# Performance work log

Hardware: AMD Instinct MI355X
Metric: run time of the kernel (lower is better)

Reference implementation:

```python
import jax, jax.numpy as jnp
import numpy as np

B, N = 4, 2048
NUM_SHAPES = 16
EPS = 1e-5


def _angle(u, v):
    # u, v: [b, 3, n] -> angle via atan2(||u x v||, u.v), standard PPF angle
    s = jnp.linalg.norm(jnp.cross(u, v, axis=1), axis=1)
    c = jnp.sum(u * v, axis=1)
    return jnp.arctan2(s, c)


def _ppf(p1, p2, n1, n2):
    d = p2 - p1  # [b,3,n]
    return jnp.stack([_angle(n1, d), _angle(n2, d), _angle(n1, n2),
                      jnp.linalg.norm(d, axis=1)], axis=1)  # [b,4,n]


def _smlp(x, w, g, b):
    # 1x1 Conv1d (no bias; absorbed by BN) + BatchNorm1d (batch stats) + ReLU
    y = jnp.einsum('oc,bcn->bon', w, x)
    mu = y.mean(axis=(0, 2), keepdims=True)
    var = jnp.mean((y - mu) ** 2, axis=(0, 2), keepdims=True)
    y = (y - mu) * jax.lax.rsqrt(var + EPS) * g[None, :, None] + b[None, :, None]
    return jax.nn.relu(y)


def _forward(inputs, pf0_w, pf0_g, pf0_b, pf1_w, pf1_g, pf1_b,
             pf2_w, pf2_g, pf2_b, pf3_w, pf3_g, pf3_b,
             cls0_w, cls0_g, cls0_b, cls1_w, cls1_g, cls1_b,
             cls2_w, cls2_g, cls2_b, cls3_w, cls3_bias):
    one_hot = inputs[:, -NUM_SHAPES:, :]
    coords = inputs[:, :3, :]
    n = coords.shape[2]
    normals = inputs[:, 3:6, :]
    normals = normals / jnp.linalg.norm(normals, axis=1, keepdims=True)

    cc = coords.mean(axis=2, keepdims=True)          # [b,3,1]
    cn = normals.mean(axis=2, keepdims=True)         # [b,3,1]
    ncn = cn / jnp.linalg.norm(cn, axis=1, keepdims=True)

    old_ppfs = _ppf(jnp.broadcast_to(cc, coords.shape), coords,
                    jnp.broadcast_to(cn, coords.shape), normals)  # [b,4,n]

    nc = coords - cc
    dot = jnp.sum(nc * ncn, axis=1, keepdims=True)   # [b,1,n]
    proj = nc - dot * cn                              # [b,3,n] (unnormalized cn, as in source)
    P = proj.transpose(0, 2, 1)                       # [b,n,3]

    cos_a = jnp.einsum('bic,bjc->bij', P, P)          # [b,n,n]
    sin_a = jnp.linalg.norm(jnp.cross(P[:, :, None, :], P[:, None, :, :]), axis=-1)
    at = jnp.arctan2(sin_a, cos_a)
    at = jnp.where(at <= 1e-5, jnp.float32(100.0), at)
    # torch.median -> lower median: sorted index (n-1)//2
    alpha = jnp.sort(at, axis=2)[:, :, (n - 1) // 2]  # [b,n]

    feats = jnp.concatenate([old_ppfs, alpha[:, None, :]], axis=1)  # [b,5,n]

    outs = [one_hot]
    f = feats
    for w, g, b in [(pf0_w, pf0_g, pf0_b), (pf1_w, pf1_g, pf1_b),
                    (pf2_w, pf2_g, pf2_b), (pf3_w, pf3_g, pf3_b)]:
        f = _smlp(f, w, g, b)
        outs.append(f)
    outs.append(jnp.broadcast_to(jnp.max(f, axis=-1, keepdims=True), f.shape))
    x = jnp.concatenate(outs, axis=1)                 # [b,2384,n]

    for w, g, b in [(cls0_w, cls0_g, cls0_b), (cls1_w, cls1_g, cls1_b),
                    (cls2_w, cls2_g, cls2_b)]:
        x = _smlp(x, w, g, b)
    return jnp.einsum('oc,bcn->bon', cls3_w, x) + cls3_bias[None, :, None]


def setup_inputs() -> dict:
    key = jax.random.key(0)
    ks = jax.random.split(key, 12)
    inp = {"inputs": jax.random.normal(ks[0], (B, 3 + 3 + NUM_SHAPES, N), jnp.float32)}
    pf_dims = [(5, 64), (64, 128), (128, 128), (128, 1024)]
    for i, (ci, co) in enumerate(pf_dims):
        inp[f"pf{i}_w"] = jax.random.normal(ks[1 + i], (co, ci), jnp.float32) / np.sqrt(ci).astype(np.float32)
        inp[f"pf{i}_g"] = jnp.ones((co,), jnp.float32)
        inp[f"pf{i}_b"] = jnp.zeros((co,), jnp.float32)
    cls_dims = [(2384, 256), (256, 256), (256, 128)]
    for j, (ci, co) in enumerate(cls_dims):
        inp[f"cls{j}_w"] = jax.random.normal(ks[6 + j], (co, ci), jnp.float32) / np.sqrt(ci).astype(np.float32)
        inp[f"cls{j}_g"] = jnp.ones((co,), jnp.float32)
        inp[f"cls{j}_b"] = jnp.zeros((co,), jnp.float32)
    inp["cls3_w"] = jax.random.normal(ks[10], (50, 128), jnp.float32) / np.sqrt(128).astype(np.float32)
    inp["cls3_bias"] = jnp.zeros((50,), jnp.float32)
    return inp


def reference(inputs, pf0_w, pf0_g, pf0_b, pf1_w, pf1_g, pf1_b,
              pf2_w, pf2_g, pf2_b, pf3_w, pf3_g, pf3_b,
              cls0_w, cls0_g, cls0_b, cls1_w, cls1_g, cls1_b,
              cls2_w, cls2_g, cls2_b, cls3_w, cls3_bias):
    return _forward(inputs, pf0_w, pf0_g, pf0_b, pf1_w, pf1_g, pf1_b,
                    pf2_w, pf2_g, pf2_b, pf3_w, pf3_g, pf3_b,
                    cls0_w, cls0_g, cls0_b, cls1_w, cls1_g, cls1_b,
                    cls2_w, cls2_g, cls2_b, cls3_w, cls3_bias)
```

## Files before the change

### kernel.cpp

```cpp
#include <hip/hip_runtime.h>
#include <math.h>

#define BB 4
#define NN 2048
#define MM 8192
#define EPSF 1e-5f
#define LDC 1376

typedef _Float16 half8 __attribute__((ext_vector_type(8)));
typedef float f32x4 __attribute__((ext_vector_type(4)));

__device__ __forceinline__ unsigned short f2h(float x) {
    _Float16 h = (_Float16)x;
    return __builtin_bit_cast(unsigned short, h);
}
__device__ __forceinline__ float h2f(unsigned short u) {
    return (float)__builtin_bit_cast(_Float16, u);
}
__device__ __forceinline__ unsigned fflip(float x) {
    unsigned u = __builtin_bit_cast(unsigned, x);
    return (u >> 31) ? ~u : (u | 0x80000000u);
}
__device__ __forceinline__ float funflip(unsigned s) {
    unsigned u = (s >> 31) ? (s ^ 0x80000000u) : ~s;
    return __builtin_bit_cast(float, u);
}
#define FLIP_NEG_INF 0x007FFFFFu

__device__ __forceinline__ int wave_sum_dpp(int v) {
    v += __builtin_amdgcn_update_dpp(0, v, 0x111, 0xF, 0xF, true);
    v += __builtin_amdgcn_update_dpp(0, v, 0x112, 0xF, 0xF, true);
    v += __builtin_amdgcn_update_dpp(0, v, 0x114, 0xF, 0xF, true);
    v += __builtin_amdgcn_update_dpp(0, v, 0x118, 0xF, 0xF, true);
    v += __builtin_amdgcn_update_dpp(0, v, 0x142, 0xa, 0xF, true);
    v += __builtin_amdgcn_update_dpp(0, v, 0x143, 0xc, 0xF, true);
    return __builtin_amdgcn_readlane(v, 63);
}

__device__ __forceinline__ float angle3(float ux, float uy, float uz,
                                        float vx, float vy, float vz) {
    float crx = uy * vz - uz * vy;
    float cry = uz * vx - ux * vz;
    float crz = ux * vy - uy * vx;
    float s = sqrtf(crx * crx + cry * cry + crz * crz);
    float c = ux * vx + uy * vy + uz * vz;
    return atan2f(s, c);
}

__device__ __forceinline__ void bncoef(const float* __restrict__ sums,
                                       const float* __restrict__ g,
                                       const float* __restrict__ bb,
                                       int o, float& a, float& c) {
    float mu = sums[o] * (1.f / 8192.f);
    float var = sums[1024 + o] * (1.f / 8192.f) - mu * mu;
    var = fmaxf(var, 0.f);
    a = g[o] * (1.0f / sqrtf(var + EPSF));
    c = bb[o] - mu * a;
}

__global__ __launch_bounds__(256) void prep_k(const float* __restrict__ in,
                                              const float* __restrict__ w1, const float* __restrict__ w2,
                                              const float* __restrict__ w3, const float* __restrict__ w4,
                                              const float* __restrict__ w5, const float* __restrict__ w6,
                                              const float* __restrict__ w7,
                                              unsigned short* __restrict__ Wb,
                                              float* __restrict__ st,
                                              unsigned* __restrict__ zp,
                                              unsigned short* __restrict__ XCb) {
    int blk = blockIdx.x;
    int t = threadIdx.x;
    if (blk < 864) {
        int idx0 = blk * 1024 + t * 4;
        ushort4 r;
        unsigned short* rp = (unsigned short*)&r;
        #pragma unroll
        for (int e = 0; e < 4; ++e) {
            int idx = idx0 + e;
            unsigned short v;
            if (idx < 8192) v = f2h(w1[idx]);
            else if (idx < 24576) v = f2h(w2[idx - 8192]);
            else if (idx < 155648) v = f2h(w3[idx - 24576]);
            else if (idx < 507904) {
                int l = idx - 155648;
                int o = l / 1376, k = l - o * 1376;
                v = (k < 1360) ? f2h(w4[o * 2384 + k]) : (unsigned short)0;
            } else if (idx < 573440) v = f2h(w5[idx - 507904]);
            else if (idx < 606208) v = f2h(w6[idx - 573440]);
            else if (idx < 614400) {
                int l = idx - 606208;
                int o = l >> 7, k = l & 127;
                v = (o < 50) ? f2h(w7[o * 128 + k]) : (unsigned short)0;
            } else {
                int l = idx - 614400;
                int c = l >> 8, o = l & 255;
                v = (c < 1024) ? f2h(w4[o * 2384 + 1360 + c]) : (unsigned short)0;
            }
            rp[e] = v;
        }
        *(ushort4*)&Wb[idx0] = r;
    } else if (blk < 868) {
        int b = blk - 864;
        const float* base = in + (size_t)b * 22 * NN;
        float cs0 = 0.f, cs1 = 0.f, cs2 = 0.f, ns0 = 0.f, ns1 = 0.f, ns2 = 0.f;
        for (int n = t; n < NN; n += 256) {
            float cx = base[0 * NN + n], cy = base[1 * NN + n], cz = base[2 * NN + n];
            float nx = base[3 * NN + n], ny = base[4 * NN + n], nz = base[5 * NN + n];
            float inv = 1.0f / sqrtf(nx * nx + ny * ny + nz * nz);
            cs0 += cx; cs1 += cy; cs2 += cz;
            ns0 += nx * inv; ns1 += ny * inv; ns2 += nz * inv;
        }
        __shared__ float red[6][256];
        red[0][t] = cs0; red[1][t] = cs1; red[2][t] = cs2;
        red[3][t] = ns0; red[4][t] = ns1; red[5][t] = ns2;
        __syncthreads();
        for (int s = 128; s > 0; s >>= 1) {
            if (t < s) {
                #pragma unroll
                for (int i = 0; i < 6; ++i) red[i][t] += red[i][t + s];
            }
            __syncthreads();
        }
        if (t == 0) {
            float ccx = red[0][0] / (float)NN, ccy = red[1][0] / (float)NN, ccz = red[2][0] / (float)NN;
            float cnx = red[3][0] / (float)NN, cny = red[4][0] / (float)NN, cnz = red[5][0] / (float)NN;
            float inv = 1.0f / sqrtf(cnx * cnx + cny * cny + cnz * cnz);
            float* s9 = st + b * 16;
            s9[0] = ccx; s9[1] = ccy; s9[2] = ccz;
            s9[3] = cnx; s9[4] = cny; s9[5] = cnz;
            s9[6] = cnx * inv; s9[7] = cny * inv; s9[8] = cnz * inv;
        }
    } else if (blk < 944) {
        int idx = (blk - 868) * 256 + t;
        zp[idx] = (idx >= 14336 && idx < 18432) ? FLIP_NEG_INF : 0u;
    } else {
        int m = (blk - 944) * 256 + t;
        int b = m >> 11, n = m & (NN - 1);
        const float* src = in + (size_t)b * 22 * NN + 6 * NN + n;
        unsigned short vals[16];
        #pragma unroll
        for (int r = 0; r < 16; ++r) vals[r] = f2h(src[(size_t)r * NN]);
        ushort4* dst = (ushort4*)&XCb[(size_t)m * LDC];
        #pragma unroll
        for (int q = 0; q < 4; ++q)
            dst[q] = make_ushort4(vals[4 * q], vals[4 * q + 1], vals[4 * q + 2], vals[4 * q + 3]);
        ushort4 z = make_ushort4(0, 0, 0, 0);
        ushort4* pz = (ushort4*)&XCb[(size_t)m * LDC + 1360];
        pz[0] = z; pz[1] = z; pz[2] = z; pz[3] = z;
    }
}

__global__ __launch_bounds__(256) void point_k(const float* __restrict__ in,
                                               const float* __restrict__ st,
                                               float4* __restrict__ PQ,
                                               float* __restrict__ F0) {
    int idx = blockIdx.x * 256 + threadIdx.x;
    int b = idx >> 11, n = idx & (NN - 1);
    const float* base = in + (size_t)b * 22 * NN;
    const float* s9 = st + b * 16;
    float cx = base[0 * NN + n], cy = base[1 * NN + n], cz = base[2 * NN + n];
    float nx = base[3 * NN + n], ny = base[4 * NN + n], nz = base[5 * NN + n];
    float inv = 1.0f / sqrtf(nx * nx + ny * ny + nz * nz);
    nx *= inv; ny *= inv; nz *= inv;
    float ccx = s9[0], ccy = s9[1], ccz = s9[2];
    float cnx = s9[3], cny = s9[4], cnz = s9[5];
    float ex = s9[6], ey = s9[7], ez = s9[8];
    float dx = cx - ccx, dy = cy - ccy, dz = cz - ccz;
    F0[0 * MM + idx] = angle3(cnx, cny, cnz, dx, dy, dz);
    F0[1 * MM + idx] = angle3(nx, ny, nz, dx, dy, dz);
    F0[2 * MM + idx] = angle3(cnx, cny, cnz, nx, ny, nz);
    F0[3 * MM + idx] = sqrtf(dx * dx + dy * dy + dz * dz);
    float dot = dx * ex + dy * ey + dz * ez;
    float px = dx - dot * cnx;
    float py = dy - dot * cny;
    float pz = dz - dot * cnz;
    PQ[idx] = make_float4(px, py, pz, sqrtf(px * px + py * py + pz * pz));
}

__global__ __launch_bounds__(256) void alpha_k(const float4* __restrict__ PQ,
                                               float* __restrict__ F0) {
    int row = blockIdx.x * 4 + (threadIdx.x >> 6);
    int lane = threadIdx.x & 63;
    int b = row >> 11;
    const float4* base = PQ + (size_t)b * NN;
    float4 a = base[row & (NN - 1)];
    unsigned u[16];
    #pragma unroll
    for (int c = 0; c < 4; ++c) {
        #pragma unroll
        for (int j = 0; j < 4; ++j) {
            int s2 = c * 8 + j * 2;
            float4 bv0 = base[s2 * 64 + lane];
            float4 bv1 = base[(s2 + 1) * 64 + lane];
            float k0, k1;
            {
                float cx = a.y * bv0.z - a.z * bv0.y;
                float cy = a.z * bv0.x - a.x * bv0.z;
                float cz = a.x * bv0.y - a.y * bv0.x;
                float ss = cx * cx + cy * cy + cz * cz;
                float dc = a.x * bv0.x + a.y * bv0.y + a.z * bv0.z;
                float den = dc + a.w * bv0.w;
                float rc = __builtin_amdgcn_rcpf(den);
                k0 = ss * rc * rc;
                if (k0 <= 2.5e-11f) k0 = __builtin_inff();
            }
            {
                float cx = a.y * bv1.z - a.z * bv1.y;
                float cy = a.z * bv1.x - a.x * bv1.z;
                float cz = a.x * bv1.y - a.y * bv1.x;
                float ss = cx * cx + cy * cy + cz * cz;
                float dc = a.x * bv1.x + a.y * bv1.y + a.z * bv1.z;
                float den = dc + a.w * bv1.w;
                float rc = __builtin_amdgcn_rcpf(den);
                k1 = ss * rc * rc;
                if (k1 <= 2.5e-11f) k1 = __builtin_inff();
            }
            u[c * 4 + j] = (unsigned)f2h(k0) | ((unsigned)f2h(k1) << 16);
        }
        asm volatile("" ::: "memory");
    }
    unsigned T = 0u;
    for (int bit = 14; bit >= 0; --bit) {
        unsigned c = T | (1u << bit);
        int s0 = 0, s1 = 0;
        #pragma unroll
        for (int q = 0; q < 8; ++q) {
            s0 += (int)__popcll(__ballot((u[8 + q] & 0xFFFFu) < c));
            s1 += (int)__popcll(__ballot((u[8 + q] >> 16) < c));
        }
        int v0 = 0, v1 = 0;
        #pragma unroll
        for (int q = 0; q < 8; ++q) {
            v0 += (int)((u[q] & 0xFFFFu) < c);
            v1 += (int)((u[q] >> 16) < c);
        }
        int vsum = wave_sum_dpp(v0 + v1);
        if (vsum + s0 + s1 <= 1023) T = c;
    }
    if (lane == 0) {
        float lo = h2f((unsigned short)T);
        float hi = h2f((unsigned short)(T + 1));
        F0[4 * MM + row] = 2.0f * atanf(sqrtf(0.5f * (lo + hi)));
    }
}

__global__ __launch_bounds__(256) void pf0s_k(const float* __restrict__ F0,
                                              const float* __restrict__ W,
                                              unsigned short* __restrict__ dst,
                                              float* __restrict__ sums) {
    __shared__ float ws[320];
    int t = threadIdx.x;
    for (int i = t; i < 320; i += 256) ws[i] = W[i];
    __syncthreads();
    int ol = t & 63, mg = t >> 6;
    int m0 = blockIdx.x * 512;
    float w0 = ws[ol * 5], w1 = ws[ol * 5 + 1], w2 = ws[ol * 5 + 2], w3 = ws[ol * 5 + 3], w4 = ws[ol * 5 + 4];
    float s = 0.f, q = 0.f;
    for (int i = 0; i < 128; ++i) {
        int m = m0 + i * 4 + mg;
        float y = w0 * F0[m] + w1 * F0[MM + m] + w2 * F0[2 * MM + m]
                + w3 * F0[3 * MM + m] + w4 * F0[4 * MM + m];
        dst[(size_t)m * LDC + ol] = f2h(y);
        s += y; q += y * y;
    }
    __shared__ float ls[4][64], lq[4][64];
    ls[mg][ol] = s; lq[mg][ol] = q;
    __syncthreads();
    if (mg == 0) {
        s = ls[0][ol] + ls[1][ol] + ls[2][ol] + ls[3][ol];
        q = lq[0][ol] + lq[1][ol] + lq[2][ol] + lq[3][ol];
        atomicAdd(&sums[ol], s);
        atomicAdd(&sums[1024 + ol], q);
    }
}

template<int MODE, int TRANS, int DOMAX>
__global__ __launch_bounds__(256) void mgemm3_k(const unsigned short* __restrict__ X, int ldx,
                                                const unsigned short* __restrict__ W, int ldw,
                                                unsigned short* __restrict__ Yh, int yld, int Co, int K, int kchunk,
                                                float* __restrict__ sums,
                                                const float* __restrict__ xs, const float* __restrict__ xg,
                                                const float* __restrict__ xb,
                                                const float4* __restrict__ AB4,
                                                unsigned* __restrict__ maxbu) {
    __shared__ unsigned short As[64 * 32];
    __shared__ unsigned short Bs[128 * 32];
    __shared__ float4 ABl[352];
    int t = threadIdx.x;
    int mBase = blockIdx.x * 64;
    int oBase = blockIdx.y * 128;
    int k0c = blockIdx.z * kchunk;
    int k1c = k0c + kchunk; if (k1c > K) k1c = K;
    if (TRANS == 1) {
        float* abf = (float*)ABl;
        for (int i = t; i < K; i += 256) {
            float a, c; bncoef(xs, xg, xb, i, a, c);
            abf[2 * i] = a; abf[2 * i + 1] = c;
        }
    } else if (TRANS == 2) {
        for (int i = t; i < k1c - k0c; i += 256) ABl[i] = AB4[k0c + i];
    }
    int lane = t & 63, w = t >> 6;
    int warpM = (w & 1) * 32, warpO = (w >> 1) * 64;
    f32x4 acc[2][4];
    #pragma unroll
    for (int i = 0; i < 2; ++i)
        #pragma unroll
        for (int j = 0; j < 4; ++j) acc[i][j] = (f32x4){0.f, 0.f, 0.f, 0.f};
    int lr = t >> 2;
    int lc = (t & 3) * 8;
    const unsigned short* Xp = X + (size_t)(mBase + lr) * ldx + lc;
    const unsigned short* Wp0 = W + (size_t)(oBase + lr) * ldw + lc;
    const unsigned short* Wp1 = W + (size_t)(oBase + lr + 64) * ldw + lc;
    int ar0 = (warpM + (lane & 15)) * 32 + (lane >> 4) * 8;
    int br0 = (warpO + (lane & 15)) * 32 + (lane >> 4) * 8;
    uint4 xa = *(const uint4*)(Xp + k0c);
    uint4 wb0 = *(const uint4*)(Wp0 + k0c);
    uint4 wb1 = *(const uint4*)(Wp1 + k0c);
    for (int k = k0c; k < k1c; k += 32) {
        __syncthreads();
        uint4 xc = xa;
        if (TRANS == 1) {
            const float* abf = (const float*)ABl;
            unsigned short* p = (unsigned short*)&xc;
            int kb = k + lc;
            #pragma unroll
            for (int e = 0; e < 8; ++e)
                p[e] = f2h(fmaxf(abf[2 * (kb + e)] * h2f(p[e]) + abf[2 * (kb + e) + 1], 0.f));
        } else if (TRANS == 2) {
            unsigned short* p = (unsigned short*)&xc;
            int kb = k + lc - k0c;
            #pragma unroll
            for (int e = 0; e < 8; ++e) {
                float4 qd = ABl[kb + e];
                p[e] = f2h(fmaxf(qd.x * h2f(p[e]) + qd.y, qd.z));
            }
        }
        *(uint4*)&As[lr * 32 + lc] = xc;
        *(uint4*)&Bs[lr * 32 + lc] = wb0;
        *(uint4*)&Bs[(lr + 64) * 32 + lc] = wb1;
        if (k + 32 < k1c) {
            xa = *(const uint4*)(Xp + k + 32);
            wb0 = *(const uint4*)(Wp0 + k + 32);
            wb1 = *(const uint4*)(Wp1 + k + 32);
        }
        __syncthreads();
        half8 a0 = __builtin_bit_cast(half8, *(const uint4*)&As[ar0]);
        half8 a1 = __builtin_bit_cast(half8, *(const uint4*)&As[ar0 + 16 * 32]);
        half8 b0 = __builtin_bit_cast(half8, *(const uint4*)&Bs[br0]);
        half8 b1 = __builtin_bit_cast(half8, *(const uint4*)&Bs[br0 + 16 * 32]);
        half8 b2 = __builtin_bit_cast(half8, *(const uint4*)&Bs[br0 + 32 * 32]);
        half8 b3 = __builtin_bit_cast(half8, *(const uint4*)&Bs[br0 + 48 * 32]);
        acc[0][0] = __builtin_amdgcn_mfma_f32_16x16x32_f16(a0, b0, acc[0][0], 0, 0, 0);
        acc[0][1] = __builtin_amdgcn_mfma_f32_16x16x32_f16(a0, b1, acc[0][1], 0, 0, 0);
        acc[0][2] = __builtin_amdgcn_mfma_f32_16x16x32_f16(a0, b2, acc[0][2], 0, 0, 0);
        acc[0][3] = __builtin_amdgcn_mfma_f32_16x16x32_f16(a0, b3, acc[0][3], 0, 0, 0);
        acc[1][0] = __builtin_amdgcn_mfma_f32_16x16x32_f16(a1, b0, acc[1][0], 0, 0, 0);
        acc[1][1] = __builtin_amdgcn_mfma_f32_16x16x32_f16(a1, b1, acc[1][1], 0, 0, 0);
        acc[1][2] = __builtin_amdgcn_mfma_f32_16x16x32_f16(a1, b2, acc[1][2], 0, 0, 0);
        acc[1][3] = __builtin_amdgcn_mfma_f32_16x16x32_f16(a1, b3, acc[1][3], 0, 0, 0);
    }
    unsigned short* Yp = Yh + (MODE == 2 ? (size_t)blockIdx.z * MM * yld : 0);
    #pragma unroll
    for (int i = 0; i < 2; ++i)
        #pragma unroll
        for (int j = 0; j < 4; ++j) {
            int m0 = mBase + warpM + i * 16 + (lane >> 4) * 4;
            int o = oBase + warpO + j * 16 + (lane & 15);
            #pragma unroll
            for (int r = 0; r < 4; ++r)
                Yp[(size_t)(m0 + r) * yld + o] = f2h(acc[i][j][r]);
        }
    if (MODE == 1) {
        __syncthreads();
        float* ssum = (float*)As;
        unsigned* smax = (unsigned*)As + 128;
        float* ssq = (float*)Bs;
        if (t < 128) { ssum[t] = 0.f; ssq[t] = 0.f; if (DOMAX) smax[t] = FLIP_NEG_INF; }
        __syncthreads();
        #pragma unroll
        for (int j = 0; j < 4; ++j) {
            int oc = warpO + j * 16 + (lane & 15);
            float s = 0.f, q = 0.f, mx = -__builtin_inff();
            #pragma unroll
            for (int i = 0; i < 2; ++i)
                #pragma unroll
                for (int r = 0; r < 4; ++r) {
                    float v = acc[i][j][r];
                    s += v; q += v * v; mx = fmaxf(mx, v);
                }
            atomicAdd(&ssum[oc], s);
            atomicAdd(&ssq[oc], q);
            if (DOMAX) atomicMax(&smax[oc], fflip(mx));
        }
        __syncthreads();
        if (t < 128) {
            atomicAdd(&sums[oBase + t], ssum[t]);
            atomicAdd(&sums[1024 + oBase + t], ssq[t]);
            if (DOMAX) atomicMax(&maxbu[(mBase >> 11) * 1024 + oBase + t], smax[t]);
        }
    }
}

template<int MODE, int TRANS>
__global__ __launch_bounds__(256) void mgemm64_k(const unsigned short* __restrict__ X, int ldx,
                                                 const unsigned short* __restrict__ W, int ldw,
                                                 void* __restrict__ Yv, int yld, int Co, int K,
                                                 float* __restrict__ sums,
                                                 const float* __restrict__ xs, const float* __restrict__ xg,
                                                 const float* __restrict__ xb) {
    __shared__ unsigned short As[64 * 32];
    __shared__ unsigned short Bs[64 * 32];
    __shared__ float ABl[512];
    int t = threadIdx.x;
    int mBase = blockIdx.x * 64;
    int oBase = blockIdx.y * 64;
    if (TRANS == 1) {
        for (int i = t; i < K; i += 256) {
            float a, c; bncoef(xs, xg, xb, i, a, c);
            ABl[2 * i] = a; ABl[2 * i + 1] = c;
        }
    }
    int lane = t & 63, w = t >> 6;
    int warpM = (w & 1) * 32, warpO = (w >> 1) * 32;
    f32x4 acc[2][2];
    #pragma unroll
    for (int i = 0; i < 2; ++i)
        #pragma unroll
        for (int j = 0; j < 2; ++j) acc[i][j] = (f32x4){0.f, 0.f, 0.f, 0.f};
    int lr = t >> 2;
    int lc = (t & 3) * 8;
    const unsigned short* Xp = X + (size_t)(mBase + lr) * ldx + lc;
    const unsigned short* Wp = W + (size_t)(oBase + lr) * ldw + lc;
    int ar0 = (warpM + (lane & 15)) * 32 + (lane >> 4) * 8;
    int br0 = (warpO + (lane & 15)) * 32 + (lane >> 4) * 8;
    uint4 xa = *(const uint4*)(Xp);
    uint4 wb = *(const uint4*)(Wp);
    for (int k = 0; k < K; k += 32) {
        __syncthreads();
        uint4 xc = xa;
        if (TRANS == 1) {
            unsigned short* p = (unsigned short*)&xc;
            int kb = k + lc;
            #pragma unroll
            for (int e = 0; e < 8; ++e)
                p[e] = f2h(fmaxf(ABl[2 * (kb + e)] * h2f(p[e]) + ABl[2 * (kb + e) + 1], 0.f));
        }
        *(uint4*)&As[lr * 32 + lc] = xc;
        *(uint4*)&Bs[lr * 32 + lc] = wb;
        if (k + 32 < K) {
            xa = *(const uint4*)(Xp + k + 32);
            wb = *(const uint4*)(Wp + k + 32);
        }
        __syncthreads();
        half8 a0 = __builtin_bit_cast(half8, *(const uint4*)&As[ar0]);
        half8 a1 = __builtin_bit_cast(half8, *(const uint4*)&As[ar0 + 16 * 32]);
        half8 b0 = __builtin_bit_cast(half8, *(const uint4*)&Bs[br0]);
        half8 b1 = __builtin_bit_cast(half8, *(const uint4*)&Bs[br0 + 16 * 32]);
        acc[0][0] = __builtin_amdgcn_mfma_f32_16x16x32_f16(a0, b0, acc[0][0], 0, 0, 0);
        acc[0][1] = __builtin_amdgcn_mfma_f32_16x16x32_f16(a0, b1, acc[0][1], 0, 0, 0);
        acc[1][0] = __builtin_amdgcn_mfma_f32_16x16x32_f16(a1, b0, acc[1][0], 0, 0, 0);
        acc[1][1] = __builtin_amdgcn_mfma_f32_16x16x32_f16(a1, b1, acc[1][1], 0, 0, 0);
    }
    if (MODE == 3) {
        float* outp = (float*)Yv;
        #pragma unroll
        for (int i = 0; i < 2; ++i)
            #pragma unroll
            for (int j = 0; j < 2; ++j) {
                int m0 = mBase + warpM + i * 16 + (lane >> 4) * 4;
                int o = oBase + warpO + j * 16 + (lane & 15);
                if (o < 50) {
                    int bb2 = m0 >> 11, n = m0 & (NN - 1);
                    float bi = sums[o];
                    float4 v = make_float4(acc[i][j][0] + bi, acc[i][j][1] + bi,
                                           acc[i][j][2] + bi, acc[i][j][3] + bi);
                    *(float4*)&outp[((size_t)bb2 * 50 + o) * NN + n] = v;
                }
            }
    } else {
        unsigned short* Yh = (unsigned short*)Yv;
        #pragma unroll
        for (int i = 0; i < 2; ++i)
            #pragma unroll
            for (int j = 0; j < 2; ++j) {
                int m0 = mBase + warpM + i * 16 + (lane >> 4) * 4;
                int o = oBase + warpO + j * 16 + (lane & 15);
                #pragma unroll
                for (int r = 0; r < 4; ++r)
                    Yh[(size_t)(m0 + r) * yld + o] = f2h(acc[i][j][r]);
            }
        __syncthreads();
        float* ssum = (float*)As;
        float* ssq = (float*)Bs;
        if (t < 64) { ssum[t] = 0.f; ssq[t] = 0.f; }
        __syncthreads();
        #pragma unroll
        for (int j = 0; j < 2; ++j) {
            int oc = warpO + j * 16 + (lane & 15);
            float s = 0.f, q = 0.f;
            #pragma unroll
            for (int i = 0; i < 2; ++i)
                #pragma unroll
                for (int r = 0; r < 4; ++r) { float v = acc[i][j][r]; s += v; q += v * v; }
            atomicAdd(&ssum[oc], s);
            atomicAdd(&ssq[oc], q);
        }
        __syncthreads();
        if (t < 64) {
            atomicAdd(&sums[oBase + t], ssum[t]);
            atomicAdd(&sums[1024 + oBase + t], ssq[t]);
        }
    }
}

__global__ __launch_bounds__(256) void abgemv_k(const float* __restrict__ SUMS,
                                                const unsigned* __restrict__ MAXBu,
                                                float4* __restrict__ AB4,
                                                const unsigned short* __restrict__ Wmax,
                                                float* __restrict__ contrib,
                                                const float* g0, const float* b0,
                                                const float* g1, const float* b1,
                                                const float* g2, const float* b2,
                                                const float* g3, const float* b3) {
    int blk = blockIdx.x, t = threadIdx.x;
    if (blk < 6) {
        int ch = blk * 256 + t;
        if (ch >= 1376) return;
        float4 r;
        if (ch < 16) r = make_float4(1.f, 0.f, -__builtin_inff(), 0.f);
        else if (ch < 80) { float a, c; bncoef(SUMS, g0, b0, ch - 16, a, c); r = make_float4(a, c, 0.f, 0.f); }
        else if (ch < 208) { float a, c; bncoef(SUMS + 2048, g1, b1, ch - 80, a, c); r = make_float4(a, c, 0.f, 0.f); }
        else if (ch < 336) { float a, c; bncoef(SUMS + 4096, g2, b2, ch - 208, a, c); r = make_float4(a, c, 0.f, 0.f); }
        else if (ch < 1360) { float a, c; bncoef(SUMS + 6144, g3, b3, ch - 336, a, c); r = make_float4(a, c, 0.f, 0.f); }
        else r = make_float4(0.f, 0.f, 0.f, 0.f);
        AB4[ch] = r;
    } else {
        int i = blk - 6;
        int b = i >> 3;
        int cc = (i & 7) * 128;
        __shared__ float nm[128];
        if (t < 128) {
            int c = cc + t;
            float a, cf; bncoef(SUMS + 6144, g3, b3, c, a, cf);
            float raw = funflip(MAXBu[b * 1024 + c]);
            nm[t] = fmaxf(a * raw + cf, 0.f);
        }
        __syncthreads();
        int o = t;
        float acc = 0.f;
        for (int c = 0; c < 128; ++c)
            acc += h2f(Wmax[(size_t)(cc + c) * 256 + o]) * nm[c];
        atomicAdd(&contrib[b * 256 + o], acc);
    }
}

__global__ __launch_bounds__(256) void red4stat_k(unsigned short* __restrict__ Yh,
                                                  const float* __restrict__ contrib,
                                                  float* __restrict__ sums) {
    int o0 = blockIdx.x * 64;
    int m0 = blockIdx.y * 128;
    int t = threadIdx.x, ol = t & 63, mg = t >> 6;
    int b = m0 >> 11;
    float cb = contrib[b * 256 + o0 + ol];
    const size_t stride = (size_t)MM * 256;
    float s = 0.f, q = 0.f;
    unsigned short* p = Yh + (size_t)(m0 + mg) * 256 + o0 + ol;
    for (int i = 0; i < 32; ++i) {
        unsigned short* pp = p + (size_t)i * 4 * 256;
        float v = h2f(pp[0]) + h2f(pp[stride]) + h2f(pp[2 * stride]) + h2f(pp[3 * stride]) + cb;
        pp[0] = f2h(v);
        s += v; q += v * v;
    }
    __shared__ float ls[4][64], lq[4][64];
    ls[mg][ol] = s; lq[mg][ol] = q;
    __syncthreads();
    if (mg == 0) {
        s = ls[0][ol] + ls[1][ol] + ls[2][ol] + ls[3][ol];
        q = lq[0][ol] + lq[1][ol] + lq[2][ol] + lq[3][ol];
        atomicAdd(&sums[o0 + ol], s);
        atomicAdd(&sums[1024 + o0 + ol], q);
    }
}

extern "C" void kernel_launch(void* const* d_in, const int* in_sizes, int n_in,
                              void* d_out, int out_size, void* d_ws, size_t ws_size,
                              hipStream_t stream) {
    const float* in = (const float*)d_in[0];
    const float* pf0_w = (const float*)d_in[1];
    const float* pf_g[4] = {(const float*)d_in[2], (const float*)d_in[5], (const float*)d_in[8], (const float*)d_in[11]};
    const float* pf_b[4] = {(const float*)d_in[3], (const float*)d_in[6], (const float*)d_in[9], (const float*)d_in[12]};
    const float* pf_w[4] = {(const float*)d_in[1], (const float*)d_in[4], (const float*)d_in[7], (const float*)d_in[10]};
    const float* cls_w[3] = {(const float*)d_in[13], (const float*)d_in[16], (const float*)d_in[19]};
    const float* cls_g[3] = {(const float*)d_in[14], (const float*)d_in[17], (const float*)d_in[20]};
    const float* cls_b[3] = {(const float*)d_in[15], (const float*)d_in[18], (const float*)d_in[21]};
    const float* cls3_w = (const float*)d_in[22];
    const float* cls3_bias = (const float*)d_in[23];
    float* out = (float*)d_out;

    char* wsb = (char*)d_ws;
    float* ST = (float*)(wsb + 0);
    float4* PQ = (float4*)(wsb + 256);
    float* F0 = (float*)(wsb + 131328);
    float* SUMS = (float*)(wsb + 295168);
    unsigned* MAXBu = (unsigned*)(wsb + 352512);
    float* CONTRIB = (float*)(wsb + 368896);
    float4* AB4 = (float4*)(wsb + 372992);
    unsigned short* WB = (unsigned short*)(wsb + 411392);
    unsigned short* XCb = (unsigned short*)(wsb + 2180864);
    unsigned short* C1b = (unsigned short*)(wsb + 24725248);
    unsigned short* C2b = (unsigned short*)(wsb + 28919552);
    unsigned short* Yh = (unsigned short*)(wsb + 33113856);

    auto SL = [&](int s) { return SUMS + (size_t)s * 2048; };

    prep_k<<<976, 256, 0, stream>>>(in, pf_w[1], pf_w[2], pf_w[3], cls_w[0], cls_w[1], cls_w[2], cls3_w,
                                    WB, ST, (unsigned*)SUMS, XCb);
    point_k<<<MM / 256, 256, 0, stream>>>(in, ST, PQ, F0);
    alpha_k<<<MM / 4, 256, 0, stream>>>(PQ, F0);

    pf0s_k<<<16, 256, 0, stream>>>(F0, pf0_w, XCb + 16, SL(0));
    mgemm64_k<1, 1><<<dim3(128, 2), 256, 0, stream>>>(XCb + 16, LDC, WB, 64, XCb + 80, LDC, 128, 64,
                                                      SL(1), SL(0), pf_g[0], pf_b[0]);
    mgemm64_k<1, 1><<<dim3(128, 2), 256, 0, stream>>>(XCb + 80, LDC, WB + 8192, 128, XCb + 208, LDC, 128, 128,
                                                      SL(2), SL(1), pf_g[1], pf_b[1]);
    mgemm3_k<1, 1, 1><<<dim3(128, 8, 1), 256, 0, stream>>>(XCb + 208, LDC, WB + 24576, 128, XCb + 336, LDC,
                                                           1024, 128, 128, SL(3), SL(2), pf_g[2], pf_b[2],
                                                           AB4, MAXBu);
    abgemv_k<<<38, 256, 0, stream>>>(SUMS, MAXBu, AB4, WB + 614400, CONTRIB,
                                     pf_g[0], pf_b[0], pf_g[1], pf_b[1], pf_g[2], pf_b[2], pf_g[3], pf_b[3]);
    mgemm3_k<2, 2, 0><<<dim3(128, 2, 4), 256, 0, stream>>>(XCb, LDC, WB + 155648, 1376, Yh, 256,
                                                           256, 1376, 352, SL(4), nullptr, nullptr, nullptr,
                                                           AB4, MAXBu);
    red4stat_k<<<dim3(4, 64), 256, 0, stream>>>(Yh, CONTRIB, SL(4));
    mgemm64_k<1, 1><<<dim3(128, 4), 256, 0, stream>>>(Yh, 256, WB + 507904, 256, C1b, 256, 256, 256,
                                                      SL(5), SL(4), cls_g[0], cls_b[0]);
    mgemm64_k<1, 1><<<dim3(128, 2), 256, 0, stream>>>(C1b, 256, WB + 507904 + 65536, 256, C2b, 128, 128, 256,
                                                      SL(6), SL(5), cls_g[1], cls_b[1]);
    mgemm64_k<3, 1><<<dim3(128, 1), 256, 0, stream>>>(C2b, 128, WB + 606208, 128, (void*)out, 0, 64, 128,
                                                      (float*)cls3_bias, SL(6), cls_g[2], cls_b[2]);

    (void)in_sizes; (void)n_in; (void)out_size; (void)ws_size;
}
```

Before: 178.6 us.

## Replace bitwise radix-select median with two-pass LDS histogram select

```diff
diff --git a/kernel.cpp b/kernel.cpp
--- a/kernel.cpp
+++ b/kernel.cpp
@@ -26,16 +26,6 @@
     return __builtin_bit_cast(float, u);
 }
 #define FLIP_NEG_INF 0x007FFFFFu
-
-__device__ __forceinline__ int wave_sum_dpp(int v) {
-    v += __builtin_amdgcn_update_dpp(0, v, 0x111, 0xF, 0xF, true);
-    v += __builtin_amdgcn_update_dpp(0, v, 0x112, 0xF, 0xF, true);
-    v += __builtin_amdgcn_update_dpp(0, v, 0x114, 0xF, 0xF, true);
-    v += __builtin_amdgcn_update_dpp(0, v, 0x118, 0xF, 0xF, true);
-    v += __builtin_amdgcn_update_dpp(0, v, 0x142, 0xa, 0xF, true);
-    v += __builtin_amdgcn_update_dpp(0, v, 0x143, 0xc, 0xF, true);
-    return __builtin_amdgcn_readlane(v, 63);
-}
 
 __device__ __forceinline__ float angle3(float ux, float uy, float uz,
                                         float vx, float vy, float vz) {
@@ -178,8 +168,10 @@
 
 __global__ __launch_bounds__(256) void alpha_k(const float4* __restrict__ PQ,
                                                float* __restrict__ F0) {
-    int row = blockIdx.x * 4 + (threadIdx.x >> 6);
+    __shared__ unsigned hist[4][256];
+    int wv = threadIdx.x >> 6;
     int lane = threadIdx.x & 63;
+    int row = blockIdx.x * 4 + wv;
     int b = row >> 11;
     const float4* base = PQ + (size_t)b * NN;
     float4 a = base[row & (NN - 1)];
@@ -218,24 +210,64 @@
         }
         asm volatile("" ::: "memory");
     }
-    unsigned T = 0u;
-    for (int bit = 14; bit >= 0; --bit) {
-        unsigned c = T | (1u << bit);
-        int s0 = 0, s1 = 0;
-        #pragma unroll
-        for (int q = 0; q < 8; ++q) {
-            s0 += (int)__popcll(__ballot((u[8 + q] & 0xFFFFu) < c));
-            s1 += (int)__popcll(__ballot((u[8 + q] >> 16) < c));
-        }
-        int v0 = 0, v1 = 0;
-        #pragma unroll
-        for (int q = 0; q < 8; ++q) {
-            v0 += (int)((u[q] & 0xFFFFu) < c);
-            v1 += (int)((u[q] >> 16) < c);
-        }
-        int vsum = wave_sum_dpp(v0 + v1);
-        if (vsum + s0 + s1 <= 1023) T = c;
-    }
+    unsigned* h = hist[wv];
+    h[lane] = 0; h[lane + 64] = 0; h[lane + 128] = 0; h[lane + 192] = 0;
+    __syncthreads();
+    #pragma unroll
+    for (int q = 0; q < 16; ++q) {
+        atomicAdd(&h[(u[q] & 0xFFFFu) >> 7], 1u);
+        atomicAdd(&h[u[q] >> 23], 1u);
+    }
+    __syncthreads();
+    const unsigned K = 1023;
+    unsigned h0 = h[4 * lane], h1 = h[4 * lane + 1], h2 = h[4 * lane + 2], h3 = h[4 * lane + 3];
+    unsigned lsum = h0 + h1 + h2 + h3;
+    unsigned inc = lsum;
+    #pragma unroll
+    for (int d = 1; d < 64; d <<= 1) {
+        unsigned tv = __shfl_up(inc, d);
+        if (lane >= d) inc += tv;
+    }
+    unsigned excl = inc - lsum;
+    bool has = (excl <= K) && (K < inc);
+    unsigned long long mask = __ballot(has);
+    int L = __ffsll((long long)mask) - 1;
+    unsigned packed = 0;
+    if (has) {
+        unsigned e = excl, Bq = 4 * lane;
+        if (e + h0 <= K) { e += h0; Bq++;
+            if (e + h1 <= K) { e += h1; Bq++;
+                if (e + h2 <= K) { e += h2; Bq++; } } }
+        packed = (Bq << 16) | e;
+    }
+    packed = __shfl(packed, L);
+    unsigned B = packed >> 16;
+    unsigned k2 = K - (packed & 0xFFFFu);
+    __syncthreads();
+    h[lane] = 0; h[lane + 64] = 0;
+    __syncthreads();
+    #pragma unroll
+    for (int q = 0; q < 16; ++q) {
+        unsigned lo = u[q] & 0xFFFFu, hi = u[q] >> 16;
+        if ((lo >> 7) == B) atomicAdd(&h[lo & 127], 1u);
+        if ((hi >> 7) == B) atomicAdd(&h[hi & 127], 1u);
+    }
+    __syncthreads();
+    unsigned g0 = h[2 * lane], g1 = h[2 * lane + 1];
+    unsigned ls2 = g0 + g1, inc2 = ls2;
+    #pragma unroll
+    for (int d = 1; d < 64; d <<= 1) {
+        unsigned tv = __shfl_up(inc2, d);
+        if (lane >= d) inc2 += tv;
+    }
+    unsigned excl2 = inc2 - ls2;
+    bool has2 = (excl2 <= k2) && (k2 < inc2);
+    unsigned long long m2 = __ballot(has2);
+    int L2 = __ffsll((long long)m2) - 1;
+    unsigned low = 0;
+    if (has2) low = 2 * lane + ((excl2 + g0 <= k2) ? 1u : 0u);
+    low = __shfl(low, L2);
+    unsigned T = (B << 7) | low;
     if (lane == 0) {
         float lo = h2f((unsigned short)T);
         float hi = h2f((unsigned short)(T + 1));
```

After: 164.4 us. 7.9% less time.
